# Performance work log

Hardware: AMD Instinct MI355X
Metric: run time of the kernel (lower is better)

The kernel has to match this reference:

```python
import jax, jax.numpy as jnp
import numpy as np

B, N, DIM = 4, 2048, 1024
HEADS, DHEAD = 16, 64
INNER = HEADS * DHEAD  # 1024


def _sigma(t):
    # elu(x) + 1 feature map (strictly positive)
    return jax.nn.elu(t) + 1.0


def setup_inputs() -> dict:
    key = jax.random.key(0)
    k1, k2, k3, k4, k5 = jax.random.split(key, 5)
    x = jax.random.normal(k1, (B, N, DIM), dtype=jnp.float32)
    M = jax.random.normal(k2, (B, HEADS, DHEAD, DHEAD), dtype=jnp.float32)
    Z = jnp.ones((B, HEADS, DHEAD, 1), dtype=jnp.float32)
    W_qkv = jax.random.normal(k3, (DIM, 3 * INNER), dtype=jnp.float32) * (DIM ** -0.5)
    beta_lin = jnp.ones((1,), dtype=jnp.float32) * 4.6     # Linear_Attention.beta
    beta_gate = jax.random.normal(k4, (1, HEADS, 1, 1), dtype=jnp.float32)  # per-head gate
    return {"x": x, "M": M, "Z": Z, "W_qkv": W_qkv, "beta_lin": beta_lin, "beta_gate": beta_gate}


def reference(x, M, Z, W_qkv, beta_lin, beta_gate):
    b, n, _ = x.shape
    scale = DHEAD ** -0.5

    qkv = x @ W_qkv                                   # [b, n, 3*inner]
    q, k, v = jnp.split(qkv, 3, axis=-1)
    # b n (h d) -> b h n d
    to_heads = lambda t: t.reshape(b, n, HEADS, DHEAD).transpose(0, 2, 1, 3)
    q, k, v = to_heads(q), to_heads(k), to_heads(v)

    # ---- linear-attention compressive memory branch ----
    sq = _sigma(q)                                    # [b h n d]
    sk = _sigma(k)
    A_mem = jnp.einsum('bhnd,bhdv->bhnv', sq, M) / jnp.einsum('bhnd,bhdi->bhni', sq, Z)
    moment = jnp.einsum('bhnd,bhdv->bhnv', sk, M) / jnp.einsum('bhnd,bhdi->bhni', sk, Z)

    # EMA state update (training path)
    beta_m = jnp.clip(jax.nn.sigmoid(beta_lin), 0.9, 0.999)  # scalar in (0.9, 0.999)
    Z_new = beta_m * Z + jnp.sum(sk, axis=-2)[..., None]      # [b h d 1]
    M_new = beta_m * M + jnp.einsum('bhnd,bhnv->bhdv', sk, v - moment)

    # ---- standard dot-product attention branch ----
    dots = jnp.einsum('bhid,bhjd->bhij', q, k) * scale
    attn = jax.nn.softmax(dots, axis=-1)
    A_dot = jnp.einsum('bhij,bhjd->bhid', attn, v)

    # ---- learned per-head gate ----
    g = jax.nn.sigmoid(beta_gate)                     # [1 h 1 1]
    A = g * A_mem + (1.0 - g) * A_dot                 # [b h n d]
    A = A.transpose(0, 2, 1, 3).reshape(b, n, INNER)  # b h n d -> b n (h d)
    return (A, M_new, Z_new)
```

## Files before the change

kernel.cpp:

```cpp
#include <hip/hip_runtime.h>
#include <math.h>

#define B_ 4
#define N_ 2048
#define DIM_ 1024
#define H_ 16
#define D_ 64
#define INNER_ 1024
#define BH_ (B_*H_)

#define A_ELEMS  (B_*N_*INNER_)
#define M_ELEMS  (BH_*D_*D_)
#define Z_ELEMS  (BH_*D_)

#define SC_LOG2E 0.18033688011112042f

typedef __attribute__((ext_vector_type(8))) short short8;
typedef __attribute__((ext_vector_type(4))) float f32x4;
typedef __attribute__((ext_vector_type(4))) unsigned short us4;
typedef unsigned short u16;

typedef const unsigned int __attribute__((address_space(1))) gu32;
typedef unsigned int __attribute__((address_space(3))) su32;

__device__ __forceinline__ u16 f2bf(float f) {
    unsigned int u = __float_as_uint(f);
    u += 0x7fffu + ((u >> 16) & 1u);
    return (u16)(u >> 16);
}
__device__ __forceinline__ float bf2f(u16 s) {
    return __uint_as_float(((unsigned int)s) << 16);
}
__device__ __forceinline__ float sigma_f(float x) {
    return x > 0.f ? x + 1.f : __expf(x);
}
__device__ __forceinline__ short8 sig8(short8 in) {
    short8 out;
    u16* ip = (u16*)&in; u16* op = (u16*)&out;
    #pragma unroll
    for (int c = 0; c < 8; c++) op[c] = f2bf(sigma_f(bf2f(ip[c])));
    return out;
}

__global__ __launch_bounds__(256) void cvt_x(const float* __restrict__ x,
                                             u16* __restrict__ xb) {
    long i = ((long)blockIdx.x * 256 + threadIdx.x) * 4;
    float4 f = *(const float4*)&x[i];
    us4 o = {f2bf(f.x), f2bf(f.y), f2bf(f.z), f2bf(f.w)};
    *(us4*)&xb[i] = o;
}

__global__ __launch_bounds__(256) void cvt_w(const float* __restrict__ W,
                                             u16* __restrict__ Wt) {
    __shared__ u16 T[64 * 68];
    const int t  = threadIdx.x;
    const int n0 = blockIdx.x * 64, k0 = blockIdx.y * 64;
    #pragma unroll
    for (int i = 0; i < 4; i++) {
        int r  = (t >> 4) + i * 16;
        int c4 = (t & 15) * 4;
        float4 f = *(const float4*)&W[(long)(k0 + r) * 3072 + n0 + c4];
        T[(c4 + 0) * 68 + r] = f2bf(f.x);
        T[(c4 + 1) * 68 + r] = f2bf(f.y);
        T[(c4 + 2) * 68 + r] = f2bf(f.z);
        T[(c4 + 3) * 68 + r] = f2bf(f.w);
    }
    __syncthreads();
    #pragma unroll
    for (int i = 0; i < 4; i++) {
        int n  = (t >> 4) + i * 16;
        int k4 = (t & 15) * 4;
        us4 o;
        o.x = T[n * 68 + k4];     o.y = T[n * 68 + k4 + 1];
        o.z = T[n * 68 + k4 + 2]; o.w = T[n * 68 + k4 + 3];
        *(us4*)&Wt[(long)(n0 + n) * 1024 + k0 + k4] = o;
    }
}

__global__ __launch_bounds__(256) void qkv_mfma(
    const u16* __restrict__ xb, const u16* __restrict__ Wt,
    u16* __restrict__ q, u16* __restrict__ k, u16* __restrict__ v) {
    __shared__ u16 As[2][128 * 32];
    __shared__ u16 Bs[2][128 * 32];
    const int t = threadIdx.x, w = t >> 6, lane = t & 63;
    const int quad = lane >> 4, l16 = lane & 15;

    const int lin = blockIdx.x;
    const int wg  = (lin & 7) * 192 + (lin >> 3);
    const int j0  = (wg % 24) * 128;
    const int m0  = (wg / 24) * 128;
    const int mw = (w >> 1) * 64, nw = (w & 1) * 64;

    const int srow = t >> 2;
    const int scol = (t & 3) * 8;

    f32x4 acc[4][4] = {};

    #pragma unroll
    for (int i = 0; i < 2; i++) {
        int r = srow + i * 64;
        __builtin_amdgcn_global_load_lds(
            (gu32*)&xb[(long)(m0 + r) * 1024 + scol],
            (su32*)&As[0][r * 32 + scol], 16, 0, 0);
        __builtin_amdgcn_global_load_lds(
            (gu32*)&Wt[(long)(j0 + r) * 1024 + scol],
            (su32*)&Bs[0][r * 32 + scol], 16, 0, 0);
    }
    __syncthreads();

    for (int kt = 0; kt < 32; ++kt) {
        const int cur = kt & 1;
        if (kt + 1 < 32) {
            const int nxt = cur ^ 1;
            const int k0 = (kt + 1) * 32;
            #pragma unroll
            for (int i = 0; i < 2; i++) {
                int r = srow + i * 64;
                __builtin_amdgcn_global_load_lds(
                    (gu32*)&xb[(long)(m0 + r) * 1024 + k0 + scol],
                    (su32*)&As[nxt][r * 32 + scol], 16, 0, 0);
                __builtin_amdgcn_global_load_lds(
                    (gu32*)&Wt[(long)(j0 + r) * 1024 + k0 + scol],
                    (su32*)&Bs[nxt][r * 32 + scol], 16, 0, 0);
            }
        }

        short8 af[4], bf[4];
        #pragma unroll
        for (int mt = 0; mt < 4; mt++)
            af[mt] = *(const short8*)&As[cur][(mw + mt * 16 + l16) * 32 + quad * 8];
        #pragma unroll
        for (int nt = 0; nt < 4; nt++)
            bf[nt] = *(const short8*)&Bs[cur][(nw + nt * 16 + l16) * 32 + quad * 8];
        #pragma unroll
        for (int mt = 0; mt < 4; mt++)
            #pragma unroll
            for (int nt = 0; nt < 4; nt++)
                acc[mt][nt] = __builtin_amdgcn_mfma_f32_16x16x32_bf16(
                    af[mt], bf[nt], acc[mt][nt], 0, 0, 0);

        __syncthreads();
    }

    #pragma unroll
    for (int mt = 0; mt < 4; mt++) {
        #pragma unroll
        for (int r = 0; r < 4; r++) {
            int mm = m0 + mw + mt * 16 + quad * 4 + r;
            int b  = mm >> 11, n = mm & 2047;
            #pragma unroll
            for (int nt = 0; nt < 4; nt++) {
                int col   = j0 + nw + nt * 16 + l16;
                int which = col >> 10;
                int rem   = col & 1023;
                int h = rem >> 6, d = rem & 63;
                long idx = (((long)(b * H_ + h)) * N_ + n) * D_ + d;
                u16 val = f2bf(acc[mt][nt][r]);
                u16* dst = (which == 0) ? q : (which == 1) ? k : v;
                dst[idx] = val;
            }
        }
    }
}

__global__ __launch_bounds__(256) void vt_transpose(
    const u16* __restrict__ vb, u16* __restrict__ vT) {
    __shared__ u16 T[64 * 72];
    const int bh = blockIdx.y;
    const int n0 = blockIdx.x * 64;
    const int t  = threadIdx.x;
    const int jj = t >> 3, kg = (t & 7) * 8;
    #pragma unroll
    for (int i = 0; i < 2; i++) {
        int j = jj + i * 32;
        short8 vv = *(const short8*)&vb[(((long)bh * N_ + n0 + j) << 6) + kg];
        u16* vp = (u16*)&vv;
        int jc = j ^ kg;
        #pragma unroll
        for (int c = 0; c < 8; c++) T[(kg + c) * 72 + jc] = vp[c];
    }
    __syncthreads();
    const int d = t >> 2, sg = (t & 3) * 16, xr = d & 56;
    short8 a0 = *(const short8*)&T[d * 72 + (sg ^ xr)];
    short8 a1 = *(const short8*)&T[d * 72 + ((sg + 8) ^ xr)];
    u16* dst = vT + ((long)bh * 64 + d) * 2048 + n0 + sg;
    *(short8*)dst       = a0;
    *(short8*)(dst + 8) = a1;
}

__global__ __launch_bounds__(256) void init_mz(
    const float* __restrict__ M, const float* __restrict__ Z,
    const float* __restrict__ beta_lin,
    float* __restrict__ outM, float* __restrict__ outZ) {
    float beta = 1.f / (1.f + __expf(-beta_lin[0]));
    beta = fminf(fmaxf(beta, 0.9f), 0.999f);
    int i = blockIdx.x * 256 + threadIdx.x;
    if (i < M_ELEMS) outM[i] = beta * M[i];
    if (i < Z_ELEMS) outZ[i] = beta * Z[i];
}

__global__ __launch_bounds__(256) void linear_mfma(
    const u16* __restrict__ qg, const u16* __restrict__ kg_,
    const u16* __restrict__ vTg, const float* __restrict__ Mg,
    const float* __restrict__ Zg, const float* __restrict__ beta_gate,
    float* __restrict__ outA, float* __restrict__ outM, float* __restrict__ outZ) {
    __shared__ u16 MTz[80 * 72];
    __shared__ u16 sqsh[64 * 72];
    __shared__ u16 sksh[64 * 72];
    __shared__ u16 skT[64 * 72];
    __shared__ u16 vT[64 * 72];
    __shared__ u16 vmT[80 * 72];
    __shared__ float dks[64];

    const int bh = blockIdx.y, b = bh >> 4, h = bh & 15;
    const int t = threadIdx.x, w = t >> 6, lane = t & 63;
    const int quad = lane >> 4, l16 = lane & 15;
    const long bhN = (long)bh * N_;

    #pragma unroll
    for (int i = 0; i < 4; i++) {
        int d  = (t >> 4) + i * 16;
        int c4 = (t & 15) * 4;
        float4 f = *(const float4*)&Mg[bh * 4096 + d * 64 + c4];
        MTz[(c4 + 0) * 72 + d] = f2bf(f.x);
        MTz[(c4 + 1) * 72 + d] = f2bf(f.y);
        MTz[(c4 + 2) * 72 + d] = f2bf(f.z);
        MTz[(c4 + 3) * 72 + d] = f2bf(f.w);
    }
    if (t < 64) {
        MTz[64 * 72 + t] = f2bf(Zg[bh * 64 + t]);
        vmT[64 * 72 + t] = f2bf(1.0f);
    }
    for (int e = t; e < 15 * 72; e += 256) {
        MTz[65 * 72 + e] = 0;
        vmT[65 * 72 + e] = 0;
    }
    if (t >= 64 && t < 72) { MTz[64 * 72 + t] = 0; vmT[64 * 72 + t] = 0; }

    const float g = 1.f / (1.f + __expf(-beta_gate[h]));

    f32x4 macc[5] = {};

    const int jj = t >> 3;
    const int kgp = (t & 7) * 8;
    const int srow = t >> 2;
    const int sg   = (t & 3) * 16;

    for (int c0 = 0; c0 < 256; c0 += 64) {
        const int n0c = blockIdx.x * 256 + c0;
        __syncthreads();

        #pragma unroll
        for (int i = 0; i < 2; i++) {
            int j = jj + i * 32;
            long gb = ((bhN + n0c + j) << 6) + kgp;
            short8 q8 = sig8(*(const short8*)&qg[gb]);
            short8 k8 = sig8(*(const short8*)&kg_[gb]);
            *(short8*)&sqsh[j * 72 + kgp] = q8;
            *(short8*)&sksh[j * 72 + kgp] = k8;
            u16* kp = (u16*)&k8;
            int jc = j ^ kgp;
            #pragma unroll
            for (int c = 0; c < 8; c++) skT[(kgp + c) * 72 + jc] = kp[c];
        }
        {
            const u16* vp = vTg + ((long)bh * 64 + srow) * 2048 + n0c + sg;
            *(short8*)&vT[srow * 72 + sg]     = *(const short8*)vp;
            *(short8*)&vT[srow * 72 + sg + 8] = *(const short8*)(vp + 8);
        }
        __syncthreads();

        {
            short8 a0 = *(const short8*)&sqsh[(w * 16 + l16) * 72 + quad * 8];
            short8 a1 = *(const short8*)&sqsh[(w * 16 + l16) * 72 + 32 + quad * 8];
            f32x4 am[5];
            #pragma unroll
            for (int ct = 0; ct < 5; ct++) {
                short8 b0 = *(const short8*)&MTz[(ct * 16 + l16) * 72 + quad * 8];
                short8 b1 = *(const short8*)&MTz[(ct * 16 + l16) * 72 + 32 + quad * 8];
                f32x4 acc = {};
                acc = __builtin_amdgcn_mfma_f32_16x16x32_bf16(a0, b0, acc, 0, 0, 0);
                acc = __builtin_amdgcn_mfma_f32_16x16x32_bf16(a1, b1, acc, 0, 0, 0);
                am[ct] = acc;
            }
            #pragma unroll
            for (int r = 0; r < 4; r++) {
                float dq  = __shfl(am[4][r], lane & 48, 64);
                float inv = __builtin_amdgcn_rcpf(dq);
                int n = n0c + w * 16 + quad * 4 + r;
                long row = ((long)(b * N_ + n)) * INNER_ + h * 64;
                #pragma unroll
                for (int ct = 0; ct < 4; ct++)
                    outA[row + ct * 16 + l16] = g * am[ct][r] * inv;
            }
        }

        f32x4 mt_[4];
        {
            short8 a0 = *(const short8*)&MTz[(w * 16 + l16) * 72 + quad * 8];
            short8 a1 = *(const short8*)&MTz[(w * 16 + l16) * 72 + 32 + quad * 8];
            #pragma unroll
            for (int ct = 0; ct < 4; ct++) {
                short8 b0 = *(const short8*)&sksh[(ct * 16 + l16) * 72 + quad * 8];
                short8 b1 = *(const short8*)&sksh[(ct * 16 + l16) * 72 + 32 + quad * 8];
                f32x4 acc = {};
                acc = __builtin_amdgcn_mfma_f32_16x16x32_bf16(a0, b0, acc, 0, 0, 0);
                acc = __builtin_amdgcn_mfma_f32_16x16x32_bf16(a1, b1, acc, 0, 0, 0);
                mt_[ct] = acc;
            }
            short8 z0 = *(const short8*)&MTz[(64 + l16) * 72 + quad * 8];
            short8 z1 = *(const short8*)&MTz[(64 + l16) * 72 + 32 + quad * 8];
            short8 b0 = *(const short8*)&sksh[(w * 16 + l16) * 72 + quad * 8];
            short8 b1 = *(const short8*)&sksh[(w * 16 + l16) * 72 + 32 + quad * 8];
            f32x4 acc = {};
            acc = __builtin_amdgcn_mfma_f32_16x16x32_bf16(z0, b0, acc, 0, 0, 0);
            acc = __builtin_amdgcn_mfma_f32_16x16x32_bf16(z1, b1, acc, 0, 0, 0);
            if (quad == 0) dks[w * 16 + l16] = __builtin_amdgcn_rcpf(acc[0]);
        }
        __syncthreads();

        #pragma unroll
        for (int ct = 0; ct < 4; ct++) {
            float invdk = dks[ct * 16 + l16];
            #pragma unroll
            for (int r = 0; r < 4; r++) {
                int vd = w * 16 + quad * 4 + r;
                float vv = bf2f(vT[vd * 72 + ct * 16 + l16]);
                vmT[vd * 72 + ct * 16 + l16] = f2bf(vv - mt_[ct][r] * invdk);
            }
        }
        __syncthreads();

        {
            int drow = w * 16 + l16, xr = drow & 56;
            short8 a0 = *(const short8*)&skT[drow * 72 + ((quad * 8) ^ xr)];
            short8 a1 = *(const short8*)&skT[drow * 72 + ((32 + quad * 8) ^ xr)];
            #pragma unroll
            for (int ct = 0; ct < 5; ct++) {
                short8 b0 = *(const short8*)&vmT[(ct * 16 + l16) * 72 + quad * 8];
                short8 b1 = *(const short8*)&vmT[(ct * 16 + l16) * 72 + 32 + quad * 8];
                macc[ct] = __builtin_amdgcn_mfma_f32_16x16x32_bf16(a0, b0, macc[ct], 0, 0, 0);
                macc[ct] = __builtin_amdgcn_mfma_f32_16x16x32_bf16(a1, b1, macc[ct], 0, 0, 0);
            }
        }
    }

    #pragma unroll
    for (int ct = 0; ct < 4; ct++)
        #pragma unroll
        for (int r = 0; r < 4; r++) {
            int d = w * 16 + quad * 4 + r;
            atomicAdd(&outM[bh * 4096 + d * 64 + ct * 16 + l16], macc[ct][r]);
        }
    if (l16 == 0)
        #pragma unroll
        for (int r = 0; r < 4; r++)
            atomicAdd(&outZ[bh * 64 + w * 16 + quad * 4 + r], macc[4][r]);
}

__global__ __launch_bounds__(256) void flash_mfma(
    const u16* __restrict__ qb, const u16* __restrict__ kb,
    const u16* __restrict__ vTg, const float* __restrict__ beta_gate,
    float* __restrict__ outA) {
    __shared__ u16 Ks[64 * 72];
    __shared__ u16 Vt[64 * 72];

    const int lin = blockIdx.x;
    const int wg  = (lin & 7) * 64 + (lin >> 3);
    const int bh  = wg >> 3;
    const int n0  = (wg & 7) * 256;
    const int b = bh >> 4, h = bh & 15;
    const int t = threadIdx.x, w = t >> 6, lane = t & 63;
    const int quad = lane >> 4, l16 = lane & 15;
    const long bhN = (long)bh * N_;

    const int srow = t >> 2;
    const int sg   = (t & 3) * 16;
    const int jloc = srow & 31;
    const int krow = (srow & 32) + ((jloc & 4) << 2) + ((jloc >> 3) << 2) + (jloc & 3);

    const u16* kbase  = kb + (bhN << 6);
    const u16* vtbase = vTg + (long)bh * 64 * 2048;

    short8 qf[4][2];
    #pragma unroll
    for (int mi = 0; mi < 4; mi++) {
        long qrow = bhN + n0 + w * 64 + mi * 16 + l16;
        qf[mi][0] = *(const short8*)&qb[(qrow << 6) + quad * 8];
        qf[mi][1] = *(const short8*)&qb[(qrow << 6) + 32 + quad * 8];
        #pragma unroll
        for (int z = 0; z < 2; z++) {
            u16* p = (u16*)&qf[mi][z];
            #pragma unroll
            for (int c = 0; c < 8; c++) p[c] = f2bf(bf2f(p[c]) * SC_LOG2E);
        }
    }

    const short8 onesf = {0x3F80, 0x3F80, 0x3F80, 0x3F80,
                          0x3F80, 0x3F80, 0x3F80, 0x3F80};

    short8 kr0, kr1, vr0, vr1;
    {
        const u16* kp = kbase + ((long)srow << 6) + sg;
        kr0 = *(const short8*)kp;
        kr1 = *(const short8*)(kp + 8);
        const u16* vp = vtbase + (long)srow * 2048 + sg;
        vr0 = *(const short8*)vp;
        vr1 = *(const short8*)(vp + 8);
    }

    f32x4 of[4][4] = {};
    f32x4 ol[4] = {};

    for (int j0 = 0; j0 < N_; j0 += 64) {
        __syncthreads();
        *(short8*)&Ks[krow * 72 + sg]     = kr0;
        *(short8*)&Ks[krow * 72 + sg + 8] = kr1;
        *(short8*)&Vt[srow * 72 + sg]     = vr0;
        *(short8*)&Vt[srow * 72 + sg + 8] = vr1;
        __syncthreads();

        if (j0 + 64 < N_) {
            const u16* kp = kbase + ((long)(j0 + 64 + srow) << 6) + sg;
            kr0 = *(const short8*)kp;
            kr1 = *(const short8*)(kp + 8);
            const u16* vp = vtbase + (long)srow * 2048 + j0 + 64 + sg;
            vr0 = *(const short8*)vp;
            vr1 = *(const short8*)(vp + 8);
        }

        #pragma unroll
        for (int g = 0; g < 2; g++) {
            const int rb = g * 32;
            short8 kA0 = *(const short8*)&Ks[(rb + l16) * 72 + quad * 8];
            short8 kA1 = *(const short8*)&Ks[(rb + l16) * 72 + 32 + quad * 8];
            short8 kB0 = *(const short8*)&Ks[(rb + 16 + l16) * 72 + quad * 8];
            short8 kB1 = *(const short8*)&Ks[(rb + 16 + l16) * 72 + 32 + quad * 8];
            short8 vf[4];
            #pragma unroll
            for (int nt = 0; nt < 4; nt++)
                vf[nt] = *(const short8*)&Vt[(nt * 16 + l16) * 72 + rb + quad * 8];

            #pragma unroll
            for (int mi = 0; mi < 4; mi++) {
                f32x4 st0 = {}, st1 = {};
                st0 = __builtin_amdgcn_mfma_f32_16x16x32_bf16(kA0, qf[mi][0], st0, 0, 0, 0);
                st0 = __builtin_amdgcn_mfma_f32_16x16x32_bf16(kA1, qf[mi][1], st0, 0, 0, 0);
                st1 = __builtin_amdgcn_mfma_f32_16x16x32_bf16(kB0, qf[mi][0], st1, 0, 0, 0);
                st1 = __builtin_amdgcn_mfma_f32_16x16x32_bf16(kB1, qf[mi][1], st1, 0, 0, 0);
                float p0 = __builtin_amdgcn_exp2f(st0[0]);
                float p1 = __builtin_amdgcn_exp2f(st0[1]);
                float p2 = __builtin_amdgcn_exp2f(st0[2]);
                float p3 = __builtin_amdgcn_exp2f(st0[3]);
                float p4 = __builtin_amdgcn_exp2f(st1[0]);
                float p5 = __builtin_amdgcn_exp2f(st1[1]);
                float p6 = __builtin_amdgcn_exp2f(st1[2]);
                float p7 = __builtin_amdgcn_exp2f(st1[3]);
                short8 af;
                unsigned int* au = (unsigned int*)&af;
                au[0] = __builtin_amdgcn_perm(__float_as_uint(p1), __float_as_uint(p0),
                                              0x07060302u);
                au[1] = __builtin_amdgcn_perm(__float_as_uint(p3), __float_as_uint(p2),
                                              0x07060302u);
                au[2] = __builtin_amdgcn_perm(__float_as_uint(p5), __float_as_uint(p4),
                                              0x07060302u);
                au[3] = __builtin_amdgcn_perm(__float_as_uint(p7), __float_as_uint(p6),
                                              0x07060302u);
                ol[mi] = __builtin_amdgcn_mfma_f32_16x16x32_bf16(af, onesf, ol[mi], 0, 0, 0);
                #pragma unroll
                for (int nt = 0; nt < 4; nt++)
                    of[mi][nt] = __builtin_amdgcn_mfma_f32_16x16x32_bf16(
                        af, vf[nt], of[mi][nt], 0, 0, 0);
            }
        }
    }

    const float g  = 1.f / (1.f + __expf(-beta_gate[h]));
    const float gi = 1.f - g;
    #pragma unroll
    for (int mi = 0; mi < 4; mi++) {
        #pragma unroll
        for (int r = 0; r < 4; r++) {
            float sc = gi / ol[mi][r];
            int n = n0 + w * 64 + mi * 16 + quad * 4 + r;
            #pragma unroll
            for (int nt = 0; nt < 4; nt++) {
                long idx = ((long)(b * N_ + n)) * INNER_ + h * 64 + nt * 16 + l16;
                outA[idx] += sc * of[mi][nt][r];
            }
        }
    }
}

extern "C" void kernel_launch(void* const* d_in, const int* in_sizes, int n_in,
                              void* d_out, int out_size, void* d_ws, size_t ws_size,
                              hipStream_t stream) {
    const float* x         = (const float*)d_in[0];
    const float* M         = (const float*)d_in[1];
    const float* Z         = (const float*)d_in[2];
    const float* W         = (const float*)d_in[3];
    const float* beta_lin  = (const float*)d_in[4];
    const float* beta_gate = (const float*)d_in[5];

    float* out  = (float*)d_out;
    float* outA = out;
    float* outM = out + A_ELEMS;
    float* outZ = out + A_ELEMS + M_ELEMS;

    u16* xb = (u16*)d_ws;
    u16* Wt = xb + (size_t)8192 * 1024;
    u16* qb = Wt + (size_t)3072 * 1024;
    u16* kb = qb + (size_t)BH_ * N_ * D_;
    u16* vb = kb + (size_t)BH_ * N_ * D_;
    u16* vt = vb + (size_t)BH_ * N_ * D_;

    cvt_x<<<dim3(A_ELEMS / 1024), 256, 0, stream>>>(x, xb);
    cvt_w<<<dim3(48, 16), 256, 0, stream>>>(W, Wt);
    qkv_mfma<<<dim3(1536), 256, 0, stream>>>(xb, Wt, qb, kb, vb);
    vt_transpose<<<dim3(N_ / 64, BH_), 256, 0, stream>>>(vb, vt);
    init_mz<<<dim3((M_ELEMS + 255) / 256), 256, 0, stream>>>(M, Z, beta_lin, outM, outZ);
    linear_mfma<<<dim3(8, BH_), 256, 0, stream>>>(qb, kb, vt, M, Z, beta_gate,
                                                  outA, outM, outZ);
    flash_mfma<<<dim3(N_ / 256 * BH_), 256, 0, stream>>>(qb, kb, vt, beta_gate, outA);
}
```

Baseline: 277.7 us.

## Split flash attention key tiles across two wave groups with LDS reduction

Doubles the flash attention workgroup to 512 threads. Each half of the waves handles one 32-key half of every 64-key tile for the same query rows. The partial output and row-sum accumulators are then combined through shared memory before the final gated write. This aims to raise wave count and latency hiding per CU, at the cost of extra LDS (the comb buffer), a multi-barrier reduction epilogue, and duplicated Q fragments in registers.

```diff
diff --git a/kernel.cpp b/kernel.cpp
--- a/kernel.cpp
+++ b/kernel.cpp
@@ -358,12 +358,13 @@
             atomicAdd(&outZ[bh * 64 + w * 16 + quad * 4 + r], macc[4][r]);
 }
 
-__global__ __launch_bounds__(256) void flash_mfma(
+__global__ __launch_bounds__(512, 4) void flash_mfma(
     const u16* __restrict__ qb, const u16* __restrict__ kb,
     const u16* __restrict__ vTg, const float* __restrict__ beta_gate,
     float* __restrict__ outA) {
     __shared__ u16 Ks[64 * 72];
     __shared__ u16 Vt[64 * 72];
+    __shared__ float comb[4][64][17];
 
     const int lin = blockIdx.x;
     const int wg  = (lin & 7) * 64 + (lin >> 3);
@@ -372,10 +373,13 @@
     const int b = bh >> 4, h = bh & 15;
     const int t = threadIdx.x, w = t >> 6, lane = t & 63;
     const int quad = lane >> 4, l16 = lane & 15;
+    const int wq = w & 3;
+    const int kh = w >> 2;
+    const int rb = kh * 32;
     const long bhN = (long)bh * N_;
 
-    const int srow = t >> 2;
-    const int sg   = (t & 3) * 16;
+    const int srow = t >> 3;
+    const int sg   = (t & 7) * 8;
     const int jloc = srow & 31;
     const int krow = (srow & 32) + ((jloc & 4) << 2) + ((jloc >> 3) << 2) + (jloc & 3);
 
@@ -385,7 +389,7 @@
     short8 qf[4][2];
     #pragma unroll
     for (int mi = 0; mi < 4; mi++) {
-        long qrow = bhN + n0 + w * 64 + mi * 16 + l16;
+        long qrow = bhN + n0 + wq * 64 + mi * 16 + l16;
         qf[mi][0] = *(const short8*)&qb[(qrow << 6) + quad * 8];
         qf[mi][1] = *(const short8*)&qb[(qrow << 6) + 32 + quad * 8];
         #pragma unroll
@@ -399,14 +403,10 @@
     const short8 onesf = {0x3F80, 0x3F80, 0x3F80, 0x3F80,
                           0x3F80, 0x3F80, 0x3F80, 0x3F80};
 
-    short8 kr0, kr1, vr0, vr1;
+    short8 kr0, vr0;
     {
-        const u16* kp = kbase + ((long)srow << 6) + sg;
-        kr0 = *(const short8*)kp;
-        kr1 = *(const short8*)(kp + 8);
-        const u16* vp = vtbase + (long)srow * 2048 + sg;
-        vr0 = *(const short8*)vp;
-        vr1 = *(const short8*)(vp + 8);
+        kr0 = *(const short8*)(kbase + ((long)srow << 6) + sg);
+        vr0 = *(const short8*)(vtbase + (long)srow * 2048 + sg);
     }
 
     f32x4 of[4][4] = {};
@@ -414,79 +414,100 @@
 
     for (int j0 = 0; j0 < N_; j0 += 64) {
         __syncthreads();
-        *(short8*)&Ks[krow * 72 + sg]     = kr0;
-        *(short8*)&Ks[krow * 72 + sg + 8] = kr1;
-        *(short8*)&Vt[srow * 72 + sg]     = vr0;
-        *(short8*)&Vt[srow * 72 + sg + 8] = vr1;
+        *(short8*)&Ks[krow * 72 + sg] = kr0;
+        *(short8*)&Vt[srow * 72 + sg] = vr0;
         __syncthreads();
 
         if (j0 + 64 < N_) {
-            const u16* kp = kbase + ((long)(j0 + 64 + srow) << 6) + sg;
-            kr0 = *(const short8*)kp;
-            kr1 = *(const short8*)(kp + 8);
-            const u16* vp = vtbase + (long)srow * 2048 + j0 + 64 + sg;
-            vr0 = *(const short8*)vp;
-            vr1 = *(const short8*)(vp + 8);
-        }
-
-        #pragma unroll
-        for (int g = 0; g < 2; g++) {
-            const int rb = g * 32;
-            short8 kA0 = *(const short8*)&Ks[(rb + l16) * 72 + quad * 8];
-            short8 kA1 = *(const short8*)&Ks[(rb + l16) * 72 + 32 + quad * 8];
-            short8 kB0 = *(const short8*)&Ks[(rb + 16 + l16) * 72 + quad * 8];
-            short8 kB1 = *(const short8*)&Ks[(rb + 16 + l16) * 72 + 32 + quad * 8];
-            short8 vf[4];
+            kr0 = *(const short8*)(kbase + ((long)(j0 + 64 + srow) << 6) + sg);
+            vr0 = *(const short8*)(vtbase + (long)srow * 2048 + j0 + 64 + sg);
+        }
+
+        short8 kA0 = *(const short8*)&Ks[(rb + l16) * 72 + quad * 8];
+        short8 kA1 = *(const short8*)&Ks[(rb + l16) * 72 + 32 + quad * 8];
+        short8 kB0 = *(const short8*)&Ks[(rb + 16 + l16) * 72 + quad * 8];
+        short8 kB1 = *(const short8*)&Ks[(rb + 16 + l16) * 72 + 32 + quad * 8];
+        short8 vf[4];
+        #pragma unroll
+        for (int nt = 0; nt < 4; nt++)
+            vf[nt] = *(const short8*)&Vt[(nt * 16 + l16) * 72 + rb + quad * 8];
+
+        #pragma unroll
+        for (int mi = 0; mi < 4; mi++) {
+            f32x4 st0 = {}, st1 = {};
+            st0 = __builtin_amdgcn_mfma_f32_16x16x32_bf16(kA0, qf[mi][0], st0, 0, 0, 0);
+            st0 = __builtin_amdgcn_mfma_f32_16x16x32_bf16(kA1, qf[mi][1], st0, 0, 0, 0);
+            st1 = __builtin_amdgcn_mfma_f32_16x16x32_bf16(kB0, qf[mi][0], st1, 0, 0, 0);
+            st1 = __builtin_amdgcn_mfma_f32_16x16x32_bf16(kB1, qf[mi][1], st1, 0, 0, 0);
+            float p0 = __builtin_amdgcn_exp2f(st0[0]);
+            float p1 = __builtin_amdgcn_exp2f(st0[1]);
+            float p2 = __builtin_amdgcn_exp2f(st0[2]);
+            float p3 = __builtin_amdgcn_exp2f(st0[3]);
+            float p4 = __builtin_amdgcn_exp2f(st1[0]);
+            float p5 = __builtin_amdgcn_exp2f(st1[1]);
+            float p6 = __builtin_amdgcn_exp2f(st1[2]);
+            float p7 = __builtin_amdgcn_exp2f(st1[3]);
+            short8 af;
+            unsigned int* au = (unsigned int*)&af;
+            au[0] = __builtin_amdgcn_perm(__float_as_uint(p1), __float_as_uint(p0),
+                                          0x07060302u);
+            au[1] = __builtin_amdgcn_perm(__float_as_uint(p3), __float_as_uint(p2),
+                                          0x07060302u);
+            au[2] = __builtin_amdgcn_perm(__float_as_uint(p5), __float_as_uint(p4),
+                                          0x07060302u);
+            au[3] = __builtin_amdgcn_perm(__float_as_uint(p7), __float_as_uint(p6),
+                                          0x07060302u);
+            ol[mi] = __builtin_amdgcn_mfma_f32_16x16x32_bf16(af, onesf, ol[mi], 0, 0, 0);
             #pragma unroll
             for (int nt = 0; nt < 4; nt++)
-                vf[nt] = *(const short8*)&Vt[(nt * 16 + l16) * 72 + rb + quad * 8];
-
-            #pragma unroll
-            for (int mi = 0; mi < 4; mi++) {
-                f32x4 st0 = {}, st1 = {};
-                st0 = __builtin_amdgcn_mfma_f32_16x16x32_bf16(kA0, qf[mi][0], st0, 0, 0, 0);
-                st0 = __builtin_amdgcn_mfma_f32_16x16x32_bf16(kA1, qf[mi][1], st0, 0, 0, 0);
-                st1 = __builtin_amdgcn_mfma_f32_16x16x32_bf16(kB0, qf[mi][0], st1, 0, 0, 0);
-                st1 = __builtin_amdgcn_mfma_f32_16x16x32_bf16(kB1, qf[mi][1], st1, 0, 0, 0);
-                float p0 = __builtin_amdgcn_exp2f(st0[0]);
-                float p1 = __builtin_amdgcn_exp2f(st0[1]);
-                float p2 = __builtin_amdgcn_exp2f(st0[2]);
-                float p3 = __builtin_amdgcn_exp2f(st0[3]);
-                float p4 = __builtin_amdgcn_exp2f(st1[0]);
-                float p5 = __builtin_amdgcn_exp2f(st1[1]);
-                float p6 = __builtin_amdgcn_exp2f(st1[2]);
-                float p7 = __builtin_amdgcn_exp2f(st1[3]);
-                short8 af;
-                unsigned int* au = (unsigned int*)&af;
-                au[0] = __builtin_amdgcn_perm(__float_as_uint(p1), __float_as_uint(p0),
-                                              0x07060302u);
-                au[1] = __builtin_amdgcn_perm(__float_as_uint(p3), __float_as_uint(p2),
-                                              0x07060302u);
-                au[2] = __builtin_amdgcn_perm(__float_as_uint(p5), __float_as_uint(p4),
-                                              0x07060302u);
-                au[3] = __builtin_amdgcn_perm(__float_as_uint(p7), __float_as_uint(p6),
-                                              0x07060302u);
-                ol[mi] = __builtin_amdgcn_mfma_f32_16x16x32_bf16(af, onesf, ol[mi], 0, 0, 0);
+                of[mi][nt] = __builtin_amdgcn_mfma_f32_16x16x32_bf16(
+                    af, vf[nt], of[mi][nt], 0, 0, 0);
+        }
+    }
+
+    #pragma unroll
+    for (int mi = 0; mi < 4; mi++) {
+        if (kh == 1) {
+            #pragma unroll
+            for (int nt = 0; nt < 4; nt++)
                 #pragma unroll
-                for (int nt = 0; nt < 4; nt++)
-                    of[mi][nt] = __builtin_amdgcn_mfma_f32_16x16x32_bf16(
-                        af, vf[nt], of[mi][nt], 0, 0, 0);
-            }
-        }
-    }
-
-    const float g  = 1.f / (1.f + __expf(-beta_gate[h]));
-    const float gi = 1.f - g;
-    #pragma unroll
-    for (int mi = 0; mi < 4; mi++) {
-        #pragma unroll
-        for (int r = 0; r < 4; r++) {
-            float sc = gi / ol[mi][r];
-            int n = n0 + w * 64 + mi * 16 + quad * 4 + r;
-            #pragma unroll
-            for (int nt = 0; nt < 4; nt++) {
-                long idx = ((long)(b * N_ + n)) * INNER_ + h * 64 + nt * 16 + l16;
-                outA[idx] += sc * of[mi][nt][r];
+                for (int r = 0; r < 4; r++)
+                    comb[wq][lane][nt * 4 + r] = of[mi][nt][r];
+        }
+        __syncthreads();
+        if (kh == 0) {
+            #pragma unroll
+            for (int nt = 0; nt < 4; nt++)
+                #pragma unroll
+                for (int r = 0; r < 4; r++)
+                    of[mi][nt][r] += comb[wq][lane][nt * 4 + r];
+        }
+        __syncthreads();
+    }
+    if (kh == 1) {
+        #pragma unroll
+        for (int mi = 0; mi < 4; mi++)
+            #pragma unroll
+            for (int r = 0; r < 4; r++)
+                comb[wq][lane][mi * 4 + r] = ol[mi][r];
+    }
+    __syncthreads();
+
+    if (kh == 0) {
+        const float g  = 1.f / (1.f + __expf(-beta_gate[h]));
+        const float gi = 1.f - g;
+        #pragma unroll
+        for (int mi = 0; mi < 4; mi++) {
+            #pragma unroll
+            for (int r = 0; r < 4; r++) {
+                float lt = ol[mi][r] + comb[wq][lane][mi * 4 + r];
+                float sc = gi / lt;
+                int n = n0 + wq * 64 + mi * 16 + quad * 4 + r;
+                #pragma unroll
+                for (int nt = 0; nt < 4; nt++) {
+                    long idx = ((long)(b * N_ + n)) * INNER_ + h * 64 + nt * 16 + l16;
+                    outA[idx] += sc * of[mi][nt][r];
+                }
             }
         }
     }
@@ -521,5 +542,5 @@
     init_mz<<<dim3((M_ELEMS + 255) / 256), 256, 0, stream>>>(M, Z, beta_lin, outM, outZ);
     linear_mfma<<<dim3(8, BH_), 256, 0, stream>>>(qb, kb, vt, M, Z, beta_gate,
                                                   outA, outM, outZ);
-    flash_mfma<<<dim3(N_ / 256 * BH_), 256, 0, stream>>>(qb, kb, vt, beta_gate, outA);
-}
+    flash_mfma<<<dim3(N_ / 256 * BH_), 512, 0, stream>>>(qb, kb, vt, beta_gate, outA);
+}
```

After: 567.0 us. 2.04x slower.
